# Optimization experiments

Hardware: AMD Instinct MI355X
Metric: run time of the kernel (lower is better)

Reference implementation:

```python
import jax, jax.numpy as jnp
import numpy as np

B, S, D, H = 2, 2048, 1024, 16
HD = D // H  # head_dim = 64
ROPE_BASE = 10000.0


def setup_inputs() -> dict:
    key = jax.random.key(0)
    ks = jax.random.split(key, 5)
    scale = 1.0 / np.sqrt(D)
    return {
        "x": jax.random.normal(ks[0], (B, S, D), dtype=jnp.float32),
        "Wq": jax.random.normal(ks[1], (D, D), dtype=jnp.float32) * scale,
        "Wk": jax.random.normal(ks[2], (D, D), dtype=jnp.float32) * scale,
        "Wv": jax.random.normal(ks[3], (D, D), dtype=jnp.float32) * scale,
        "Wo": jax.random.normal(ks[4], (D, D), dtype=jnp.float32) * scale,
    }


def _rotate_half(x):
    x1, x2 = x[..., : HD // 2], x[..., HD // 2:]
    return jnp.concatenate((-x2, x1), axis=-1)


def _rope_cos_sin(seq_len):
    inv_freq = 1.0 / (ROPE_BASE ** (jnp.arange(0, HD, 2, dtype=jnp.float32) / HD))
    t = jnp.arange(seq_len, dtype=jnp.float32)
    freqs = jnp.outer(t, inv_freq)          # [S, HD/2]
    emb = jnp.concatenate((freqs, freqs), -1)  # [S, HD]
    return jnp.cos(emb), jnp.sin(emb)


def reference(x, Wq, Wk, Wv, Wo):
    # projections (torch Linear: y = x @ W.T), split heads -> [B, H, S, HD]
    def proj(W):
        return (x @ W.T).reshape(B, S, H, HD).transpose(0, 2, 1, 3)

    q, k, v = proj(Wq), proj(Wk), proj(Wv)

    cos, sin = _rope_cos_sin(S)  # [S, HD] each, broadcast over B, H
    q = q * cos + _rotate_half(q) * sin
    k = k * cos + _rotate_half(k) * sin

    scale = 1.0 / np.sqrt(HD)
    scores = jnp.einsum("bhsd,bhtd->bhst", q, k) * scale  # [B,H,S,S]
    attn = jax.nn.softmax(scores, axis=-1)
    out = jnp.einsum("bhst,bhtd->bhsd", attn, v)           # [B,H,S,HD]
    out = out.transpose(0, 2, 1, 3).reshape(B, S, D)
    return out @ Wo.T
```

## Files before the change

### kernel.cpp

```cpp
#include <hip/hip_runtime.h>
#include <hip/hip_bf16.h>
#include <math.h>
#include <stdint.h>

typedef __bf16 bf16;
typedef __bf16 bf16x8 __attribute__((ext_vector_type(8)));
typedef __bf16 bf16x4 __attribute__((ext_vector_type(4)));
typedef float  f32x4  __attribute__((ext_vector_type(4)));

#define MFMA16(a,b,c) __builtin_amdgcn_mfma_f32_16x16x32_bf16((a),(b),(c),0,0,0)

static constexpr int kB  = 2;
static constexpr int kS  = 2048;
static constexpr int kD  = 1024;
static constexpr int kH  = 16;
static constexpr int kHD = 64;
static constexpr int kM  = kB * kS;
static constexpr float kExpC = 0.125f * 1.44269504f;

__device__ __forceinline__ void gl_lds16(const bf16* g, bf16* l) {
  __builtin_amdgcn_global_load_lds(
      (const __attribute__((address_space(1))) unsigned int*)g,
      (__attribute__((address_space(3))) unsigned int*)l, 16, 0, 0);
}

__global__ void cvt_all(const float* __restrict__ x,
                        const float* __restrict__ wq, const float* __restrict__ wk,
                        const float* __restrict__ wv, const float* __restrict__ wo,
                        bf16* __restrict__ xb,
                        bf16* __restrict__ wqb, bf16* __restrict__ wkb,
                        bf16* __restrict__ wvb, bf16* __restrict__ wob,
                        float2* __restrict__ rtab)
{
  const int i = blockIdx.x * 256 + threadIdx.x;
  const int NX4 = (kM * kD) / 4;
  const int NW4 = (kD * kD) / 4;
  if (i >= NX4 + 4 * NW4) {
    const int idx = i - (NX4 + 4 * NW4);
    const int s = idx >> 5, d = idx & 31;
    const float f = exp2f(-(float)d * 0.4152410118609203f);
    float sn, cs;
    sincosf((float)s * f, &sn, &cs);
    rtab[idx] = make_float2(cs, sn);
    return;
  }
  const float* src; bf16* dst; int off;
  if (i < NX4) { src = x; dst = xb; off = i; }
  else {
    const int j = i - NX4;
    const int seg = j >> 18;
    off = j & (NW4 - 1);
    src = (seg == 0) ? wq : (seg == 1) ? wk : (seg == 2) ? wv : wo;
    dst = (seg == 0) ? wqb : (seg == 1) ? wkb : (seg == 2) ? wvb : wob;
  }
  const float4 v = ((const float4*)src)[off];
  bf16x4 o = { (bf16)v.x, (bf16)v.y, (bf16)v.z, (bf16)v.w };
  ((bf16x4*)dst)[off] = o;
}

__device__ __forceinline__ void gemm_core_128(
    const bf16* __restrict__ A, const bf16* __restrict__ Bw,
    int m0, int n0, int K, bf16* smem, f32x4 acc[4][4])
{
  const int t = threadIdx.x, lane = t & 63, wave = t >> 6;
  const int wm = wave >> 1, wn = wave & 1;
  const int srow = lane >> 2;
  const int scol = (lane & 3) * 8;
  const bf16* ga0 = A  + (size_t)(m0 + wave * 16 + srow) * K + scol;
  const bf16* ga1 = ga0 + (size_t)64 * K;
  const bf16* gb0 = Bw + (size_t)(n0 + wave * 16 + srow) * K + scol;
  const bf16* gb1 = gb0 + (size_t)64 * K;
  const int woff = wave * 512;

  {
    bf16* lb = smem;
    gl_lds16(ga0, lb + woff);
    gl_lds16(ga1, lb + 2048 + woff);
    gl_lds16(gb0, lb + 4096 + woff);
    gl_lds16(gb1, lb + 6144 + woff);
  }
  int cur = 0;
  for (int k0 = 0; k0 < K; k0 += 32) {
    __syncthreads();
    if (k0 + 32 < K) {
      bf16* lb = smem + (cur ^ 1) * 8192;
      gl_lds16(ga0 + k0 + 32, lb + woff);
      gl_lds16(ga1 + k0 + 32, lb + 2048 + woff);
      gl_lds16(gb0 + k0 + 32, lb + 4096 + woff);
      gl_lds16(gb1 + k0 + 32, lb + 6144 + woff);
    }
    const bf16* aT = smem + cur * 8192;
    const bf16* bT = aT + 4096;
    bf16x8 af[4], bfr[4];
#pragma unroll
    for (int i = 0; i < 4; ++i) {
      af[i]  = *(const bf16x8*)(aT + (wm * 64 + i * 16 + (lane & 15)) * 32 + (lane >> 4) * 8);
      bfr[i] = *(const bf16x8*)(bT + (wn * 64 + i * 16 + (lane & 15)) * 32 + (lane >> 4) * 8);
    }
#pragma unroll
    for (int i = 0; i < 4; ++i)
#pragma unroll
      for (int j = 0; j < 4; ++j)
        acc[i][j] = MFMA16(af[i], bfr[j], acc[i][j]);
    cur ^= 1;
  }
}

__global__ __launch_bounds__(256, 4) void proj_qkv(
    const bf16* __restrict__ xb,
    const bf16* __restrict__ wqb, const bf16* __restrict__ wkb, const bf16* __restrict__ wvb,
    bf16* __restrict__ Qb, bf16* __restrict__ Kb, bf16* __restrict__ Vt,
    const float2* __restrict__ rtab)
{
  __shared__ __align__(16) bf16 smem[16384];
  const int z = blockIdx.z;
  const bf16* Ww = (z == 0) ? wqb : (z == 1) ? wkb : wvb;
  const int m0 = blockIdx.x * 128, n0 = blockIdx.y * 128;
  f32x4 acc[4][4] = {};
  gemm_core_128(xb, Ww, m0, n0, kD, smem, acc);

  const int lane = threadIdx.x & 63, wave = threadIdx.x >> 6;
  const int wm = wave >> 1, wn = wave & 1, quad = lane >> 4, lc = lane & 15;
  const int hh = (n0 >> 6) + wn;
  if (z == 2) {
    __syncthreads();
    const int t = threadIdx.x;
    const int row = t >> 1;
    const int coff = (t & 1) * 32;
    const int bidx = m0 >> 11;
    const int hh2 = (n0 >> 6) + (row >> 6);
    const int d = row & 63;
    bf16* vtr = smem;
#pragma unroll
    for (int p = 0; p < 2; ++p) {
      if (p) __syncthreads();
      if (wm == p) {
#pragma unroll
        for (int i = 0; i < 4; ++i)
#pragma unroll
          for (int j = 0; j < 4; ++j) {
            bf16x4 pk;
#pragma unroll
            for (int r = 0; r < 4; ++r) pk[r] = (bf16)acc[i][j][r];
            *(bf16x4*)&vtr[(wn * 64 + j * 16 + lc) * 72 + i * 16 + quad * 4] = pk;
          }
      }
      __syncthreads();
      bf16* dst = Vt + ((size_t)(bidx * kH + hh2) * kHD + d) * kS
                     + (m0 & 2047) + p * 64 + coff;
#pragma unroll
      for (int u = 0; u < 4; ++u)
        *(uint4*)(dst + u * 8) = *(const uint4*)&vtr[row * 72 + coff + u * 8];
    }
  } else {
    bf16* Op = (z == 0) ? Qb : Kb;
    const float f = (z == 0) ? kExpC : 1.0f;
#pragma unroll
    for (int j = 0; j < 2; ++j) {
      const int d = j * 16 + lc;
#pragma unroll
      for (int i = 0; i < 4; ++i)
#pragma unroll
        for (int r = 0; r < 4; ++r) {
          const int m = m0 + wm * 64 + i * 16 + quad * 4 + r;
          const int bidx = m >> 11, s = m & 2047;
          const float2 cs = rtab[s * 32 + d];
          const float v0 = acc[i][j][r], v1 = acc[i][j + 2][r];
          bf16* dst = Op + ((size_t)(bidx * kH + hh) * kS + s) * kHD;
          dst[d]      = (bf16)((v0 * cs.x - v1 * cs.y) * f);
          dst[d + 32] = (bf16)((v1 * cs.x + v0 * cs.y) * f);
        }
    }
  }
}

__global__ __launch_bounds__(256, 2) void attn(
    const bf16* __restrict__ Qb, const bf16* __restrict__ Kb,
    const bf16* __restrict__ Vt, bf16* __restrict__ Ob)
{
  __shared__ __align__(16) bf16 kT2[2][128 * 64];
  __shared__ __align__(16) bf16 vT2[2][64 * 128];
  const int t = threadIdx.x, lane = t & 63, wave = t >> 6;
  const int quad = lane >> 4, lc = lane & 15;
  const int bid = blockIdx.x;
  const int qt = (bid >> 3) & 15;
  const int bh = (bid & 7) * 4 + (bid >> 7);
  const size_t base = (size_t)bh * kS * kHD;
  const bf16* Qp = Qb + base + (size_t)qt * 128 * kHD;
  const bf16* Kp = Kb + base;
  const bf16* Vp = Vt + base;

  bf16x8 qf[2][2];
#pragma unroll
  for (int tm = 0; tm < 2; ++tm)
#pragma unroll
    for (int ks = 0; ks < 2; ++ks)
      qf[tm][ks] = *(const bf16x8*)(Qp + (wave * 32 + tm * 16 + lc) * kHD + ks * 32 + quad * 8);

  f32x4 oacc[2][4] = {};
  f32x4 lacc[2] = {};
  const bf16 one = (bf16)1.0f;
  const bf16x8 ones = { one, one, one, one, one, one, one, one };

  const bf16* kst  = Kp + (size_t)(wave * 32 + (lane >> 3)) * kHD
                        + 8 * ((lane & 7) ^ (lane >> 3));
  const bf16* vst0 = Vp + (size_t)(wave * 16 + (lane >> 4)) * kS
                        + 8 * ((lane & 15) ^ (lane >> 4));
  const bf16* vst1 = Vp + (size_t)(wave * 16 + (lane >> 4)) * kS
                        + 8 * (((lane & 15) ^ (lane >> 4)) ^ 4);
  const int ldsb = wave * 2048;

#pragma unroll
  for (int i = 0; i < 4; ++i) {
    gl_lds16(kst + (size_t)i * 8 * kHD, &kT2[0][ldsb + i * 512]);
    gl_lds16(((i & 1) ? vst1 : vst0) + (size_t)i * 4 * kS, &vT2[0][ldsb + i * 512]);
  }

  int cur = 0;
  for (int kt = 0; kt < kS / 128; ++kt) {
    __syncthreads();
    if (kt + 1 < kS / 128) {
      const bf16* kn = kst + (size_t)(kt + 1) * 128 * kHD;
      const int vo = (kt + 1) * 128;
#pragma unroll
      for (int i = 0; i < 4; ++i) {
        gl_lds16(kn + (size_t)i * 8 * kHD, &kT2[cur ^ 1][ldsb + i * 512]);
        gl_lds16(((i & 1) ? vst1 : vst0) + (size_t)i * 4 * kS + vo,
                 &vT2[cur ^ 1][ldsb + i * 512]);
      }
    }
    const bf16* kbuf = kT2[cur];
    const bf16* vbuf = vT2[cur];

    bf16x8 kf[8][2];
#pragma unroll
    for (int nk = 0; nk < 8; ++nk)
#pragma unroll
      for (int ks = 0; ks < 2; ++ks)
        kf[nk][ks] = *(const bf16x8*)&kbuf[(nk * 16 + lc) * 64
                                           + 8 * ((ks * 4 + quad) ^ (lane & 7))];

    bf16x8 pfrag[2][4];
#pragma unroll
    for (int tm = 0; tm < 2; ++tm) {
      f32x4 sc[8] = {};
#pragma unroll
      for (int nk = 0; nk < 8; ++nk) {
        sc[nk] = MFMA16(kf[nk][0], qf[tm][0], sc[nk]);
        sc[nk] = MFMA16(kf[nk][1], qf[tm][1], sc[nk]);
      }
#pragma unroll
      for (int kp = 0; kp < 4; ++kp) {
        bf16x8 p;
#pragma unroll
        for (int j = 0; j < 4; ++j) {
          p[j]     = (bf16)__builtin_amdgcn_exp2f(sc[2 * kp][j]);
          p[j + 4] = (bf16)__builtin_amdgcn_exp2f(sc[2 * kp + 1][j]);
        }
        pfrag[tm][kp] = p;
      }
    }

#pragma unroll
    for (int kp = 0; kp < 4; ++kp)
#pragma unroll
      for (int tm = 0; tm < 2; ++tm)
        lacc[tm] = MFMA16(pfrag[tm][kp], ones, lacc[tm]);

#pragma unroll
    for (int nd = 0; nd < 4; ++nd)
#pragma unroll
      for (int kp = 0; kp < 4; ++kp) {
        const int r = nd * 16 + lc;
        const bf16x4 lo = *(const bf16x4*)&vbuf[r * 128
            + (((kp * 4 + (quad >> 1)) ^ (lane & 7)) * 8 + (quad & 1) * 4)];
        const bf16x4 hi = *(const bf16x4*)&vbuf[r * 128
            + (((kp * 4 + 2 + (quad >> 1)) ^ (lane & 7)) * 8 + (quad & 1) * 4)];
        const bf16x8 vfr = __builtin_shufflevector(lo, hi, 0, 1, 2, 3, 4, 5, 6, 7);
#pragma unroll
        for (int tm = 0; tm < 2; ++tm)
          oacc[tm][nd] = MFMA16(pfrag[tm][kp], vfr, oacc[tm][nd]);
      }
    cur ^= 1;
  }

  const int b = bh >> 4, h = bh & 15;
#pragma unroll
  for (int tm = 0; tm < 2; ++tm)
#pragma unroll
    for (int r = 0; r < 4; ++r) {
      const float inv = 1.0f / lacc[tm][r];
      const int s = qt * 128 + wave * 32 + tm * 16 + quad * 4 + r;
      bf16* dst = Ob + ((size_t)(b * kS + s)) * kD + h * kHD;
#pragma unroll
      for (int nd = 0; nd < 4; ++nd)
        dst[nd * 16 + lc] = (bf16)(oacc[tm][nd][r] * inv);
    }
}

__global__ __launch_bounds__(256, 4) void out_proj(
    const bf16* __restrict__ Ab, const bf16* __restrict__ wob, float* __restrict__ Cout)
{
  __shared__ __align__(16) bf16 smem[16384];
  const int m0 = blockIdx.x * 128, n0 = blockIdx.y * 128;
  f32x4 acc[4][4] = {};
  gemm_core_128(Ab, wob, m0, n0, kD, smem, acc);
  const int lane = threadIdx.x & 63, wave = threadIdx.x >> 6;
  const int wm = wave >> 1, wn = wave & 1, quad = lane >> 4, lc = lane & 15;
#pragma unroll
  for (int i = 0; i < 4; ++i)
#pragma unroll
    for (int r = 0; r < 4; ++r) {
      const int m = m0 + wm * 64 + i * 16 + quad * 4 + r;
#pragma unroll
      for (int j = 0; j < 4; ++j)
        Cout[(size_t)m * kD + n0 + wn * 64 + j * 16 + lc] = acc[i][j][r];
    }
}

extern "C" void kernel_launch(void* const* d_in, const int* in_sizes, int n_in,
                              void* d_out, int out_size, void* d_ws, size_t ws_size,
                              hipStream_t stream)
{
  const float* x  = (const float*)d_in[0];
  const float* wq = (const float*)d_in[1];
  const float* wk = (const float*)d_in[2];
  const float* wv = (const float*)d_in[3];
  const float* wo = (const float*)d_in[4];
  float* out = (float*)d_out;

  char* ws = (char*)d_ws;
  const size_t MB = 1024 * 1024;
  if (ws_size < 57 * MB) return;
  bf16* xb  = (bf16*)(ws + 0 * MB);
  bf16* wqb = (bf16*)(ws + 8 * MB);
  bf16* wkb = (bf16*)(ws + 10 * MB);
  bf16* wvb = (bf16*)(ws + 12 * MB);
  bf16* wob = (bf16*)(ws + 14 * MB);
  bf16* Qb  = (bf16*)(ws + 16 * MB);
  bf16* Kb  = (bf16*)(ws + 24 * MB);
  bf16* Ob  = (bf16*)(ws + 40 * MB);
  float2* rtab = (float2*)(ws + 48 * MB);
  bf16* Vtp = (bf16*)(ws + 49 * MB);

  cvt_all<<<8448, 256, 0, stream>>>(x, wq, wk, wv, wo, xb, wqb, wkb, wvb, wob, rtab);
  proj_qkv<<<dim3(32, 8, 3), 256, 0, stream>>>(xb, wqb, wkb, wvb, Qb, Kb, Vtp, rtab);
  attn<<<dim3(512), 256, 0, stream>>>(Qb, Kb, Vtp, Ob);
  out_proj<<<dim3(32, 8), 256, 0, stream>>>(Ob, wob, out);
}
```

Before: 182.5 us.

## Switch attention to 32x32x16 MFMA with permlane P repack and LDS-staged output

Rewrites the attention inner loop to use 32x32x16 bf16 MFMA tiles instead of 16x16x32. Each wave now handles 32 queries as one tile, and the P fragments are repacked with v_cvt_pk_bf16 and v_permlane32_swap. The row sum moves from an extra MFMA against a ones vector to plain VALU adds plus a cross-half shuffle. The output is staged through LDS so each lane can write 16-byte global stores instead of scattered 2-byte stores. The intent is fewer MFMA instructions and LDS fragment loads, no ones-MFMA, and coalesced output writes, at the cost of more VALU adds and extra register pressure from the f32x16 accumulators.

After: 178.1 us. 2.4% less time.

```diff
diff --git a/kernel.cpp b/kernel.cpp
--- a/kernel.cpp
+++ b/kernel.cpp
@@ -7,8 +7,11 @@
 typedef __bf16 bf16x8 __attribute__((ext_vector_type(8)));
 typedef __bf16 bf16x4 __attribute__((ext_vector_type(4)));
 typedef float  f32x4  __attribute__((ext_vector_type(4)));
+typedef float  f32x16 __attribute__((ext_vector_type(16)));
+typedef unsigned int u32x4 __attribute__((ext_vector_type(4)));
 
 #define MFMA16(a,b,c) __builtin_amdgcn_mfma_f32_16x16x32_bf16((a),(b),(c),0,0,0)
+#define MFMA32(a,b,c) __builtin_amdgcn_mfma_f32_32x32x16_bf16((a),(b),(c),0,0,0)
 
 static constexpr int kB  = 2;
 static constexpr int kS  = 2048;
@@ -22,6 +25,12 @@
   __builtin_amdgcn_global_load_lds(
       (const __attribute__((address_space(1))) unsigned int*)g,
       (__attribute__((address_space(3))) unsigned int*)l, 16, 0, 0);
+}
+
+__device__ __forceinline__ unsigned cvt_pk_bf16(float lo, float hi) {
+  unsigned r;
+  asm("v_cvt_pk_bf16_f32 %0, %1, %2" : "=v"(r) : "v"(lo), "v"(hi));
+  return r;
 }
 
 __global__ void cvt_all(const float* __restrict__ x,
@@ -181,7 +190,7 @@
   __shared__ __align__(16) bf16 kT2[2][128 * 64];
   __shared__ __align__(16) bf16 vT2[2][64 * 128];
   const int t = threadIdx.x, lane = t & 63, wave = t >> 6;
-  const int quad = lane >> 4, lc = lane & 15;
+  const int l31 = lane & 31, hi = lane >> 5;
   const int bid = blockIdx.x;
   const int qt = (bid >> 3) & 15;
   const int bh = (bid & 7) * 4 + (bid >> 7);
@@ -190,17 +199,13 @@
   const bf16* Kp = Kb + base;
   const bf16* Vp = Vt + base;
 
-  bf16x8 qf[2][2];
-#pragma unroll
-  for (int tm = 0; tm < 2; ++tm)
-#pragma unroll
-    for (int ks = 0; ks < 2; ++ks)
-      qf[tm][ks] = *(const bf16x8*)(Qp + (wave * 32 + tm * 16 + lc) * kHD + ks * 32 + quad * 8);
-
-  f32x4 oacc[2][4] = {};
-  f32x4 lacc[2] = {};
-  const bf16 one = (bf16)1.0f;
-  const bf16x8 ones = { one, one, one, one, one, one, one, one };
+  bf16x8 qf[4];
+#pragma unroll
+  for (int ks = 0; ks < 4; ++ks)
+    qf[ks] = *(const bf16x8*)(Qp + (size_t)(wave * 32 + l31) * kHD + ks * 16 + hi * 8);
+
+  f32x16 oacc[2] = {};
+  float lsum = 0.f;
 
   const bf16* kst  = Kp + (size_t)(wave * 32 + (lane >> 3)) * kHD
                         + 8 * ((lane & 7) ^ (lane >> 3));
@@ -217,9 +222,10 @@
   }
 
   int cur = 0;
-  for (int kt = 0; kt < kS / 128; ++kt) {
+  const int NT = kS / 128;
+  for (int kt = 0; kt < NT; ++kt) {
     __syncthreads();
-    if (kt + 1 < kS / 128) {
+    if (kt + 1 < NT) {
       const bf16* kn = kst + (size_t)(kt + 1) * 128 * kHD;
       const int vo = (kt + 1) * 128;
 #pragma unroll
@@ -232,70 +238,69 @@
     const bf16* kbuf = kT2[cur];
     const bf16* vbuf = vT2[cur];
 
-    bf16x8 kf[8][2];
-#pragma unroll
-    for (int nk = 0; nk < 8; ++nk)
-#pragma unroll
-      for (int ks = 0; ks < 2; ++ks)
-        kf[nk][ks] = *(const bf16x8*)&kbuf[(nk * 16 + lc) * 64
-                                           + 8 * ((ks * 4 + quad) ^ (lane & 7))];
-
-    bf16x8 pfrag[2][4];
-#pragma unroll
-    for (int tm = 0; tm < 2; ++tm) {
-      f32x4 sc[8] = {};
-#pragma unroll
-      for (int nk = 0; nk < 8; ++nk) {
-        sc[nk] = MFMA16(kf[nk][0], qf[tm][0], sc[nk]);
-        sc[nk] = MFMA16(kf[nk][1], qf[tm][1], sc[nk]);
-      }
-#pragma unroll
-      for (int kp = 0; kp < 4; ++kp) {
-        bf16x8 p;
-#pragma unroll
-        for (int j = 0; j < 4; ++j) {
-          p[j]     = (bf16)__builtin_amdgcn_exp2f(sc[2 * kp][j]);
-          p[j + 4] = (bf16)__builtin_amdgcn_exp2f(sc[2 * kp + 1][j]);
-        }
-        pfrag[tm][kp] = p;
-      }
-    }
-
-#pragma unroll
-    for (int kp = 0; kp < 4; ++kp)
-#pragma unroll
-      for (int tm = 0; tm < 2; ++tm)
-        lacc[tm] = MFMA16(pfrag[tm][kp], ones, lacc[tm]);
-
-#pragma unroll
-    for (int nd = 0; nd < 4; ++nd)
-#pragma unroll
-      for (int kp = 0; kp < 4; ++kp) {
-        const int r = nd * 16 + lc;
-        const bf16x4 lo = *(const bf16x4*)&vbuf[r * 128
-            + (((kp * 4 + (quad >> 1)) ^ (lane & 7)) * 8 + (quad & 1) * 4)];
-        const bf16x4 hi = *(const bf16x4*)&vbuf[r * 128
-            + (((kp * 4 + 2 + (quad >> 1)) ^ (lane & 7)) * 8 + (quad & 1) * 4)];
-        const bf16x8 vfr = __builtin_shufflevector(lo, hi, 0, 1, 2, 3, 4, 5, 6, 7);
-#pragma unroll
-        for (int tm = 0; tm < 2; ++tm)
-          oacc[tm][nd] = MFMA16(pfrag[tm][kp], vfr, oacc[tm][nd]);
+    f32x16 sacc[4] = {};
+#pragma unroll
+    for (int knb = 0; knb < 4; ++knb)
+#pragma unroll
+      for (int ks = 0; ks < 4; ++ks) {
+        const bf16x8 kf = *(const bf16x8*)&kbuf[(knb * 32 + l31) * 64
+                                               + 8 * ((ks * 2 + hi) ^ (lane & 7))];
+        sacc[knb] = MFMA32(kf, qf[ks], sacc[knb]);
+      }
+
+    bf16x8 pfrag[8];
+#pragma unroll
+    for (int knb = 0; knb < 4; ++knb) {
+      float pe[16];
+#pragma unroll
+      for (int r = 0; r < 16; ++r) pe[r] = __builtin_amdgcn_exp2f(sacc[knb][r]);
+      lsum += (((pe[0] + pe[1]) + (pe[2] + pe[3])) + ((pe[4] + pe[5]) + (pe[6] + pe[7])))
+            + (((pe[8] + pe[9]) + (pe[10] + pe[11])) + ((pe[12] + pe[13]) + (pe[14] + pe[15])));
+#pragma unroll
+      for (int h2 = 0; h2 < 2; ++h2) {
+        unsigned a0 = cvt_pk_bf16(pe[8 * h2 + 0], pe[8 * h2 + 1]);
+        unsigned a1 = cvt_pk_bf16(pe[8 * h2 + 2], pe[8 * h2 + 3]);
+        unsigned b0 = cvt_pk_bf16(pe[8 * h2 + 4], pe[8 * h2 + 5]);
+        unsigned b1 = cvt_pk_bf16(pe[8 * h2 + 6], pe[8 * h2 + 7]);
+        asm("v_permlane32_swap_b32 %0, %1" : "+v"(a0), "+v"(b0));
+        asm("v_permlane32_swap_b32 %0, %1" : "+v"(a1), "+v"(b1));
+        u32x4 w; w.x = a0; w.y = a1; w.z = b0; w.w = b1;
+        pfrag[knb * 2 + h2] = __builtin_bit_cast(bf16x8, w);
+      }
+    }
+
+#pragma unroll
+    for (int nb = 0; nb < 2; ++nb)
+#pragma unroll
+      for (int tt = 0; tt < 8; ++tt) {
+        const bf16x8 vf = *(const bf16x8*)&vbuf[(nb * 32 + l31) * 128
+                                               + 8 * ((tt * 2 + hi) ^ (lane & 7))];
+        oacc[nb] = MFMA32(vf, pfrag[tt], oacc[nb]);
       }
     cur ^= 1;
   }
 
+  __syncthreads();
+  const float total = lsum + __shfl_xor(lsum, 32);
+  const float inv = 1.0f / total;
+  bf16* tb = &kT2[0][0] + wave * 2304;
+#pragma unroll
+  for (int nb = 0; nb < 2; ++nb)
+#pragma unroll
+    for (int rq = 0; rq < 4; ++rq) {
+      bf16x4 p4;
+#pragma unroll
+      for (int e = 0; e < 4; ++e) p4[e] = (bf16)(oacc[nb][rq * 4 + e] * inv);
+      *(bf16x4*)&tb[l31 * 72 + nb * 32 + rq * 8 + hi * 4] = p4;
+    }
+  asm volatile("s_waitcnt lgkmcnt(0)" ::: "memory");
   const int b = bh >> 4, h = bh & 15;
-#pragma unroll
-  for (int tm = 0; tm < 2; ++tm)
-#pragma unroll
-    for (int r = 0; r < 4; ++r) {
-      const float inv = 1.0f / lacc[tm][r];
-      const int s = qt * 128 + wave * 32 + tm * 16 + quad * 4 + r;
-      bf16* dst = Ob + ((size_t)(b * kS + s)) * kD + h * kHD;
-#pragma unroll
-      for (int nd = 0; nd < 4; ++nd)
-        dst[nd * 16 + lc] = (bf16)(oacc[tm][nd][r] * inv);
-    }
+  const int q = lane >> 1, hf = lane & 1;
+  const bf16* srcl = &tb[q * 72 + hf * 32];
+  bf16* dst = Ob + ((size_t)(b * kS + qt * 128 + wave * 32 + q)) * kD + h * kHD + hf * 32;
+#pragma unroll
+  for (int u = 0; u < 4; ++u)
+    *(uint4*)(dst + u * 8) = *(const uint4*)(srcl + u * 8);
 }
 
 __global__ __launch_bounds__(256, 4) void out_proj(
```
